# Performance work log

Measured on AMD Instinct MI355X. Metric: run time of the kernel, lower is better.

Reference implementation:

```python
import jax, jax.numpy as jnp
import numpy as np

KH, KW, PAD, G = 3, 3, 1, 4  # kernel, padding, deformable groups


def _bilinear_gather(xg, py, px):
    """xg: [B,G,C,Hin,Win]; py,px: [B,G,K,H,W] sample coords.
    Returns [B,G,C,K,H,W] with zero padding outside the image (mmcv semantics)."""
    B, Gd, C, Hin, Win = xg.shape
    y0 = jnp.floor(py)
    x0 = jnp.floor(px)
    wy1 = py - y0
    wx1 = px - x0
    wy0 = 1.0 - wy1
    wx0 = 1.0 - wx1
    xf = xg.reshape(B, Gd, C, Hin * Win)

    def gather(yi, xi):
        valid = (yi >= 0) & (yi < Hin) & (xi >= 0) & (xi < Win)
        yc = jnp.clip(yi, 0, Hin - 1).astype(jnp.int32)
        xc = jnp.clip(xi, 0, Win - 1).astype(jnp.int32)
        lin = (yc * Win + xc).reshape(B, Gd, 1, -1)  # [B,G,1,K*H*W]
        v = jnp.take_along_axis(xf, lin, axis=3).reshape(B, Gd, C, *yi.shape[2:])
        return v * valid[:, :, None].astype(xg.dtype)

    return (gather(y0, x0) * (wy0 * wx0)[:, :, None]
            + gather(y0, x0 + 1) * (wy0 * wx1)[:, :, None]
            + gather(y0 + 1, x0) * (wy1 * wx0)[:, :, None]
            + gather(y0 + 1, x0 + 1) * (wy1 * wx1)[:, :, None])


def setup_inputs() -> dict:
    key = jax.random.key(0)
    k1, k2, k3, k4 = jax.random.split(key, 4)
    B, Cin, Cout, H, W = 8, 256, 256, 64, 64
    x = jax.random.normal(k1, (B, Cin, H, W), dtype=jnp.float32)
    shape = jax.random.normal(k2, (B, 4, H, W), dtype=jnp.float32)
    # conv_offset: 1x1 conv, 4 -> G*2*KH*KW = 72 channels, no bias
    w_offset = jax.random.normal(k3, (G * 2 * KH * KW, 4), dtype=jnp.float32) * 0.1
    # conv_adaption: deform conv weight, no bias
    w_deform = jax.random.normal(k4, (Cout, Cin, KH, KW), dtype=jnp.float32) * 0.01
    return {"x": x, "shape": shape, "w_offset": w_offset, "w_deform": w_deform}


def reference(x, shape, w_offset, w_deform):
    B, Cin, H, W = x.shape
    Cout = w_deform.shape[0]
    K = KH * KW
    # 1x1 offset-predicting conv on detached shape
    shape = jax.lax.stop_gradient(shape)
    offset = jnp.einsum('oc,bchw->bohw', w_offset, shape)  # [B, G*2*K, H, W]
    off = offset.reshape(B, G, K, 2, H, W)  # mmcv layout: (dy, dx) per tap
    dy, dx = off[:, :, :, 0], off[:, :, :, 1]  # [B,G,K,H,W]
    # base sampling grid for each kernel tap
    ky, kx = jnp.meshgrid(jnp.arange(KH), jnp.arange(KW), indexing='ij')
    ky = ky.reshape(-1)
    kx = kx.reshape(-1)
    base_y = (ky - PAD)[:, None, None] + jnp.arange(H)[None, :, None]  # [K,H,1]
    base_x = (kx - PAD)[:, None, None] + jnp.arange(W)[None, None, :]  # [K,1,W]
    py = base_y[None, None].astype(x.dtype) + dy  # [B,G,K,H,W]
    px = base_x[None, None].astype(x.dtype) + dx
    xg = x.reshape(B, G, Cin // G, H, W)
    sampled = _bilinear_gather(xg, py, px)  # [B,G,Cpg,K,H,W]
    wr = w_deform.reshape(Cout, G, Cin // G, K)
    out = jnp.einsum('ogck,bgckhw->bohw', wr, sampled)
    return jax.nn.relu(out)
```

## Files before the change

### kernel.cpp

```cpp
#include <hip/hip_runtime.h>
#include <hip/hip_bf16.h>


#define Bn   8
#define CIN  256
#define COUT 256
#define Hn   64
#define Wn   64
#define Gn   4
#define Kn   9
#define CPG  64
#define GK   36

typedef __bf16 bf16x8 __attribute__((ext_vector_type(8)));
typedef float  f32x4  __attribute__((ext_vector_type(4)));
typedef _Float16 f16x2 __attribute__((ext_vector_type(2)));

#define SWPAD 1156
__global__ void fa_prep(const float* __restrict__ x, const float* __restrict__ w,
                        __bf16* __restrict__ xt, __bf16* __restrict__ wfrag) {
    const int bid = blockIdx.x, t = threadIdx.x;
    __shared__ __bf16 sw[16 * SWPAD];
    if (bid < 4096) {
        const int c8q = bid & 7, hwt = (bid >> 3) & 63, b = bid >> 9;
        const int hw = hwt * 64 + (t & 63);
        const int c8 = c8q * 4 + (t >> 6);
        const float* xp = x + ((size_t)(b * CIN + c8 * 8) << 12) + hw;
        bf16x8 v;
#pragma unroll
        for (int j = 0; j < 8; j++) v[j] = (__bf16)xp[(size_t)j << 12];
        *(bf16x8*)&xt[(((size_t)b << 12) + hw) * 256 + c8 * 8] = v;
    } else {
        const int mt = (bid - 4096) >> 1, gh = (bid - 4096) & 1;
        const int o0 = mt * 16, g0 = gh * 2;
        const int r = t >> 4, tr = t & 15;
        const float* wp = w + (size_t)(o0 + r) * (CIN * Kn) + g0 * (CPG * Kn);
#pragma unroll
        for (int it = 0; it < 18; it++) {
            int off = it * 64 + tr * 4;
            float4 v = *(const float4*)(wp + off);
            __bf16* d = &sw[r * SWPAD + off];
            d[0] = (__bf16)v.x; d[1] = (__bf16)v.y;
            d[2] = (__bf16)v.z; d[3] = (__bf16)v.w;
        }
        __syncthreads();
#pragma unroll
        for (int it = 0; it < 9; it++) {
            int chunk = it * 256 + t;
            int lane = chunk & 63, ks = (chunk >> 6) & 1, gkl = chunk >> 7;
            int gl = gkl / Kn, k = gkl - gl * Kn;
            int gk = g0 * Kn + gkl;
            int ol = lane & 15;
            int cbase = ks * 32 + (lane >> 4) * 8;
            bf16x8 v;
#pragma unroll
            for (int j = 0; j < 8; j++)
                v[j] = sw[ol * SWPAD + (gl * CPG + cbase + j) * Kn + k];
            *(bf16x8*)&wfrag[(((size_t)gk * 16 + mt) * 2 + ks) * 512 + lane * 8] = v;
        }
    }
}

__global__ __launch_bounds__(512, 4)
void fa_main(const __bf16* __restrict__ xt, const float* __restrict__ shp,
             const float* __restrict__ w_off, const __bf16* __restrict__ wfrag,
             float* __restrict__ out) {
    const int blk = blockIdx.x;
    const int bp = blk >> 7, h = (blk >> 1) & 63, wh = blk & 1;
    const int w0 = wh * 32;
    const int t = threadIdx.x;
    const int wid = t >> 6, lane = t & 63;
    const int col = lane & 15, quad = lane >> 4;
    const int cg = t & 7, nl = (t >> 3) & 63;

    __shared__ __align__(16) int4 s_meta[GK * 64];
    __shared__ __align__(16) __bf16 sB[2][64 * 64];
    __shared__ float s_shp[2 * 4 * 32];
    __shared__ float s_woff[GK * 8];

    if (t < 256) {
        int bb = t >> 7, c = (t >> 5) & 3, wl = t & 31;
        s_shp[t] = shp[(((bp * 2 + bb) * 4 + c) << 12) + h * Wn + w0 + wl];
    }
    for (int u = t; u < GK * 8; u += 512) s_woff[u] = w_off[u];
    __syncthreads();

    for (int i = t; i < GK * 64; i += 512) {
        int gk = i >> 6, n = i & 63;
        int bb = n >> 5, wl = n & 31;
        int g = gk / Kn, k = gk - g * Kn;
        int ky = k / 3, kx = k - ky * 3;
        float dy = 0.f, dx = 0.f;
#pragma unroll
        for (int c = 0; c < 4; c++) {
            float sv = s_shp[(bb * 4 + c) * 32 + wl];
            dy = fmaf(s_woff[gk * 8 + c],     sv, dy);
            dx = fmaf(s_woff[gk * 8 + 4 + c], sv, dx);
        }
        float py = (float)(h + ky - 1) + dy;
        float px = (float)(w0 + wl + kx - 1) + dx;
        float y0 = floorf(py), x0 = floorf(px);
        float fy = py - y0, fx = px - x0;
        int iy = (int)y0, ix = (int)x0;
        bool y0v = (unsigned)iy       < (unsigned)Hn;
        bool y1v = (unsigned)(iy + 1) < (unsigned)Hn;
        bool x0v = (unsigned)ix       < (unsigned)Wn;
        bool x1v = (unsigned)(ix + 1) < (unsigned)Wn;
        int yc0 = min(max(iy, 0), Hn - 1), yc1 = min(max(iy + 1, 0), Hn - 1);
        int xc0 = min(max(ix, 0), Wn - 1), xc1 = min(max(ix + 1, 0), Wn - 1);
        int l00 = yc0 * Wn + xc0, l01 = yc0 * Wn + xc1;
        int l10 = yc1 * Wn + xc0, l11 = yc1 * Wn + xc1;
        float wy1 = fy, wy0 = 1.f - fy, wx1 = fx, wx0 = 1.f - fx;
        float w00 = (y0v && x0v) ? wy0 * wx0 : 0.f;
        float w01 = (y0v && x1v) ? wy0 * wx1 : 0.f;
        float w10 = (y1v && x0v) ? wy1 * wx0 : 0.f;
        float w11 = (y1v && x1v) ? wy1 * wx1 : 0.f;
        f16x2 p0, p1;
        p0.x = (_Float16)w00; p0.y = (_Float16)w01;
        p1.x = (_Float16)w10; p1.y = (_Float16)w11;
        s_meta[i] = make_int4(l00 | (l01 << 16), l10 | (l11 << 16),
                              __builtin_bit_cast(int, p0),
                              __builtin_bit_cast(int, p1));
    }

    bf16x8 c4[4];
    int2   amv;

    auto issue = [&](int gk) {
        int4 mv = s_meta[gk * 64 + nl];
        amv.x = mv.z; amv.y = mv.w;
        int b = bp * 2 + (nl >> 5);
        int g = gk / Kn;
        const __bf16* base = xt + (((size_t)b << 12)) * 256 + g * CPG + cg * 8;
        c4[0] = *(const bf16x8*)(base + (size_t)(mv.x & 0xffff) * 256);
        c4[1] = *(const bf16x8*)(base + (size_t)((unsigned)mv.x >> 16) * 256);
        c4[2] = *(const bf16x8*)(base + (size_t)(mv.y & 0xffff) * 256);
        c4[3] = *(const bf16x8*)(base + (size_t)((unsigned)mv.y >> 16) * 256);
    };
    auto commit = [&](int buf) {
        f16x2 h0 = __builtin_bit_cast(f16x2, amv.x);
        f16x2 h1 = __builtin_bit_cast(f16x2, amv.y);
        float w00 = (float)h0.x, w01 = (float)h0.y;
        float w10 = (float)h1.x, w11 = (float)h1.y;
        bf16x8 r;
#pragma unroll
        for (int j = 0; j < 8; j++) {
            float v = w00 * (float)c4[0][j] + w01 * (float)c4[1][j]
                    + w10 * (float)c4[2][j] + w11 * (float)c4[3][j];
            r[j] = (__bf16)v;
        }
        *(bf16x8*)&sB[buf][(nl * 8 + (cg ^ (nl & 7))) * 8] = r;
    };

    f32x4 acc[2][4];
#pragma unroll
    for (int mt = 0; mt < 2; mt++)
#pragma unroll
        for (int nt = 0; nt < 4; nt++) acc[mt][nt] = (f32x4){0.f, 0.f, 0.f, 0.f};

    __syncthreads();

    issue(0);
    commit(0);
    issue(1);
    __syncthreads();

    for (int gk = 0; gk < GK; gk++) {
        const int buf = gk & 1;
        const __bf16* wbase = wfrag + (((size_t)gk * 16 + wid * 2) * 2) * 512;
        bf16x8 af[2][2];
#pragma unroll
        for (int ks = 0; ks < 2; ks++)
#pragma unroll
            for (int mt = 0; mt < 2; mt++)
                af[ks][mt] = *(const bf16x8*)(wbase + ((size_t)(mt * 2 + ks) * 64 + lane) * 8);
        if (gk + 1 < GK) commit(buf ^ 1);
        if (gk + 2 < GK) issue(gk + 2);
#pragma unroll
        for (int ks = 0; ks < 2; ks++) {
            bf16x8 bfv[4];
#pragma unroll
            for (int nt = 0; nt < 4; nt++) {
                int n = nt * 16 + col;
                int cq8 = ks * 4 + quad;
                bfv[nt] = *(const bf16x8*)&sB[buf][(n * 8 + (cq8 ^ (n & 7))) * 8];
            }
#pragma unroll
            for (int mt = 0; mt < 2; mt++)
#pragma unroll
                for (int nt = 0; nt < 4; nt++)
                    acc[mt][nt] = __builtin_amdgcn_mfma_f32_16x16x32_bf16(
                        af[ks][mt], bfv[nt], acc[mt][nt], 0, 0, 0);
        }
        __syncthreads();
    }

#pragma unroll
    for (int mt = 0; mt < 2; mt++)
#pragma unroll
        for (int r = 0; r < 4; r++) {
            int o = wid * 32 + mt * 16 + quad * 4 + r;
#pragma unroll
            for (int nt = 0; nt < 4; nt++) {
                int n = nt * 16 + col;
                int b = bp * 2 + (n >> 5);
                int w = w0 + (n & 31);
                out[(((size_t)(b * COUT + o)) << 12) + h * Wn + w] =
                    fmaxf(acc[mt][nt][r], 0.f);
            }
        }
}

extern "C" void kernel_launch(void* const* d_in, const int* in_sizes, int n_in,
                              void* d_out, int out_size, void* d_ws, size_t ws_size,
                              hipStream_t stream) {
    const float* x     = (const float*)d_in[0];
    const float* shp   = (const float*)d_in[1];
    const float* w_off = (const float*)d_in[2];
    const float* w_def = (const float*)d_in[3];
    float* out = (float*)d_out;
    __bf16* wfrag = (__bf16*)d_ws;
    __bf16* xt    = (__bf16*)((char*)d_ws + (2u << 20));

    fa_prep<<<4096 + 32, 256, 0, stream>>>(x, w_def, xt, wfrag);
    fa_main<<<512, 512, 0, stream>>>(xt, shp, w_off, wfrag, out);
}
```

Baseline: 146.4 us.

## Switch to fp16 with packed bilinear math, LDS-transposed prep, and reordered LDS reads

Changes the transposed input and weight fragments from bf16 to fp16. The bilinear blend now runs in packed half-precision multiply-adds instead of per-element float converts, and the MFMA becomes the f16 variant. The prep kernel's x transpose now goes through a swizzled shared-memory tile with coalesced float4 reads and 16-byte writes. The main loop hoists all B-fragment LDS reads ahead of the commit/issue step and uses 32-bit index arithmetic for gathers. Accumulating the blend in fp16 and the narrower fp16 exponent range could cost accuracy.

```diff
diff --git a/kernel.cpp b/kernel.cpp
--- a/kernel.cpp
+++ b/kernel.cpp
@@ -12,26 +12,44 @@
 #define CPG  64
 #define GK   36
 
-typedef __bf16 bf16x8 __attribute__((ext_vector_type(8)));
-typedef float  f32x4  __attribute__((ext_vector_type(4)));
+typedef float    f32x4 __attribute__((ext_vector_type(4)));
 typedef _Float16 f16x2 __attribute__((ext_vector_type(2)));
+typedef _Float16 f16x8 __attribute__((ext_vector_type(8)));
 
 #define SWPAD 1156
+#define HWT   32
 __global__ void fa_prep(const float* __restrict__ x, const float* __restrict__ w,
-                        __bf16* __restrict__ xt, __bf16* __restrict__ wfrag) {
+                        _Float16* __restrict__ xt, _Float16* __restrict__ wfrag) {
     const int bid = blockIdx.x, t = threadIdx.x;
-    __shared__ __bf16 sw[16 * SWPAD];
-    if (bid < 4096) {
-        const int c8q = bid & 7, hwt = (bid >> 3) & 63, b = bid >> 9;
-        const int hw = hwt * 64 + (t & 63);
-        const int c8 = c8q * 4 + (t >> 6);
-        const float* xp = x + ((size_t)(b * CIN + c8 * 8) << 12) + hw;
-        bf16x8 v;
-#pragma unroll
-        for (int j = 0; j < 8; j++) v[j] = (__bf16)xp[(size_t)j << 12];
-        *(bf16x8*)&xt[(((size_t)b << 12) + hw) * 256 + c8 * 8] = v;
+    __shared__ __align__(16) _Float16 spool[16 * SWPAD];
+    if (bid < 1024) {
+        _Float16* sT = spool;
+        const int b = bid >> 7, tile = bid & 127;
+        const int hw0 = tile * HWT;
+        const int s = t >> 3, hwq = t & 7;
+#pragma unroll
+        for (int it = 0; it < 8; it++) {
+            int c = it * 32 + s;
+            float4 v = *(const float4*)(x + (((size_t)(b * CIN + c)) << 12) + hw0 + hwq * 4);
+            const float* vf = (const float*)&v;
+#pragma unroll
+            for (int j = 0; j < 4; j++) {
+                int hw = hwq * 4 + j;
+                sT[hw * 256 + (c ^ (hwq << 3))] = (_Float16)vf[j];
+            }
+        }
+        __syncthreads();
+        const int cg = t & 31, hwr = t >> 5;
+#pragma unroll
+        for (int it = 0; it < 4; it++) {
+            int hw = it * 8 + hwr;
+            int q = hw >> 2;
+            f16x8 v = *(const f16x8*)&sT[hw * 256 + ((cg ^ q) << 3)];
+            *(f16x8*)&xt[(((size_t)b << 12) + hw0 + hw) * 256 + cg * 8] = v;
+        }
     } else {
-        const int mt = (bid - 4096) >> 1, gh = (bid - 4096) & 1;
+        _Float16* sw = spool;
+        const int mt = (bid - 1024) >> 1, gh = (bid - 1024) & 1;
         const int o0 = mt * 16, g0 = gh * 2;
         const int r = t >> 4, tr = t & 15;
         const float* wp = w + (size_t)(o0 + r) * (CIN * Kn) + g0 * (CPG * Kn);
@@ -39,9 +57,9 @@
         for (int it = 0; it < 18; it++) {
             int off = it * 64 + tr * 4;
             float4 v = *(const float4*)(wp + off);
-            __bf16* d = &sw[r * SWPAD + off];
-            d[0] = (__bf16)v.x; d[1] = (__bf16)v.y;
-            d[2] = (__bf16)v.z; d[3] = (__bf16)v.w;
+            _Float16* d = &sw[r * SWPAD + off];
+            d[0] = (_Float16)v.x; d[1] = (_Float16)v.y;
+            d[2] = (_Float16)v.z; d[3] = (_Float16)v.w;
         }
         __syncthreads();
 #pragma unroll
@@ -52,18 +70,18 @@
             int gk = g0 * Kn + gkl;
             int ol = lane & 15;
             int cbase = ks * 32 + (lane >> 4) * 8;
-            bf16x8 v;
+            f16x8 v;
 #pragma unroll
             for (int j = 0; j < 8; j++)
                 v[j] = sw[ol * SWPAD + (gl * CPG + cbase + j) * Kn + k];
-            *(bf16x8*)&wfrag[(((size_t)gk * 16 + mt) * 2 + ks) * 512 + lane * 8] = v;
+            *(f16x8*)&wfrag[(((size_t)gk * 16 + mt) * 2 + ks) * 512 + lane * 8] = v;
         }
     }
 }
 
 __global__ __launch_bounds__(512, 4)
-void fa_main(const __bf16* __restrict__ xt, const float* __restrict__ shp,
-             const float* __restrict__ w_off, const __bf16* __restrict__ wfrag,
+void fa_main(const _Float16* __restrict__ xt, const float* __restrict__ shp,
+             const float* __restrict__ w_off, const _Float16* __restrict__ wfrag,
              float* __restrict__ out) {
     const int blk = blockIdx.x;
     const int bp = blk >> 7, h = (blk >> 1) & 63, wh = blk & 1;
@@ -74,7 +92,7 @@
     const int cg = t & 7, nl = (t >> 3) & 63;
 
     __shared__ __align__(16) int4 s_meta[GK * 64];
-    __shared__ __align__(16) __bf16 sB[2][64 * 64];
+    __shared__ __align__(16) _Float16 sB[2][64 * 64];
     __shared__ float s_shp[2 * 4 * 32];
     __shared__ float s_woff[GK * 8];
 
@@ -123,33 +141,40 @@
                               __builtin_bit_cast(int, p1));
     }
 
-    bf16x8 c4[4];
-    int2   amv;
+    f16x8 c4[4];
+    int2  amv;
+    const unsigned nBase = ((unsigned)(bp * 2 + (nl >> 5)) << 20) + (unsigned)cg * 8u;
 
     auto issue = [&](int gk) {
         int4 mv = s_meta[gk * 64 + nl];
         amv.x = mv.z; amv.y = mv.w;
-        int b = bp * 2 + (nl >> 5);
-        int g = gk / Kn;
-        const __bf16* base = xt + (((size_t)b << 12)) * 256 + g * CPG + cg * 8;
-        c4[0] = *(const bf16x8*)(base + (size_t)(mv.x & 0xffff) * 256);
-        c4[1] = *(const bf16x8*)(base + (size_t)((unsigned)mv.x >> 16) * 256);
-        c4[2] = *(const bf16x8*)(base + (size_t)(mv.y & 0xffff) * 256);
-        c4[3] = *(const bf16x8*)(base + (size_t)((unsigned)mv.y >> 16) * 256);
+        unsigned g = (unsigned)gk / (unsigned)Kn;
+        unsigned base = nBase + g * 64u;
+        c4[0] = *(const f16x8*)(xt + base + (((unsigned)mv.x & 0xffffu) << 8));
+        c4[1] = *(const f16x8*)(xt + base + (((unsigned)mv.x >> 16)     << 8));
+        c4[2] = *(const f16x8*)(xt + base + (((unsigned)mv.y & 0xffffu) << 8));
+        c4[3] = *(const f16x8*)(xt + base + (((unsigned)mv.y >> 16)     << 8));
     };
     auto commit = [&](int buf) {
-        f16x2 h0 = __builtin_bit_cast(f16x2, amv.x);
-        f16x2 h1 = __builtin_bit_cast(f16x2, amv.y);
-        float w00 = (float)h0.x, w01 = (float)h0.y;
-        float w10 = (float)h1.x, w11 = (float)h1.y;
-        bf16x8 r;
-#pragma unroll
-        for (int j = 0; j < 8; j++) {
-            float v = w00 * (float)c4[0][j] + w01 * (float)c4[1][j]
-                    + w10 * (float)c4[2][j] + w11 * (float)c4[3][j];
-            r[j] = (__bf16)v;
-        }
-        *(bf16x8*)&sB[buf][(nl * 8 + (cg ^ (nl & 7))) * 8] = r;
+        f16x2 wv0 = __builtin_bit_cast(f16x2, amv.x);
+        f16x2 wv1 = __builtin_bit_cast(f16x2, amv.y);
+        f16x2 w00 = __builtin_shufflevector(wv0, wv0, 0, 0);
+        f16x2 w01 = __builtin_shufflevector(wv0, wv0, 1, 1);
+        f16x2 w10 = __builtin_shufflevector(wv1, wv1, 0, 0);
+        f16x2 w11 = __builtin_shufflevector(wv1, wv1, 1, 1);
+        const f16x2* a0p = (const f16x2*)&c4[0];
+        const f16x2* a1p = (const f16x2*)&c4[1];
+        const f16x2* a2p = (const f16x2*)&c4[2];
+        const f16x2* a3p = (const f16x2*)&c4[3];
+        f16x8 r;
+        f16x2* rp = (f16x2*)&r;
+#pragma unroll
+        for (int p = 0; p < 4; p++) {
+            f16x2 rv = w00 * a0p[p] + w01 * a1p[p]
+                     + w10 * a2p[p] + w11 * a3p[p];
+            rp[p] = rv;
+        }
+        *(f16x8*)&sB[buf][(nl * 8 + (cg ^ (nl & 7))) * 8] = r;
     };
 
     f32x4 acc[2][4];
@@ -167,31 +192,32 @@
 
     for (int gk = 0; gk < GK; gk++) {
         const int buf = gk & 1;
-        const __bf16* wbase = wfrag + (((size_t)gk * 16 + wid * 2) * 2) * 512;
-        bf16x8 af[2][2];
+        const _Float16* wbase = wfrag + (((size_t)gk * 16 + wid * 2) * 2) * 512;
+        f16x8 af[2][2];
 #pragma unroll
         for (int ks = 0; ks < 2; ks++)
 #pragma unroll
             for (int mt = 0; mt < 2; mt++)
-                af[ks][mt] = *(const bf16x8*)(wbase + ((size_t)(mt * 2 + ks) * 64 + lane) * 8);
-        if (gk + 1 < GK) commit(buf ^ 1);
-        if (gk + 2 < GK) issue(gk + 2);
-#pragma unroll
-        for (int ks = 0; ks < 2; ks++) {
-            bf16x8 bfv[4];
+                af[ks][mt] = *(const f16x8*)(wbase + ((size_t)(mt * 2 + ks) * 64 + lane) * 8);
+        f16x8 bfv[2][4];
+#pragma unroll
+        for (int ks = 0; ks < 2; ks++)
 #pragma unroll
             for (int nt = 0; nt < 4; nt++) {
                 int n = nt * 16 + col;
                 int cq8 = ks * 4 + quad;
-                bfv[nt] = *(const bf16x8*)&sB[buf][(n * 8 + (cq8 ^ (n & 7))) * 8];
+                bfv[ks][nt] = *(const f16x8*)&sB[buf][(n * 8 + (cq8 ^ (n & 7))) * 8];
             }
+        if (gk + 1 < GK) commit(buf ^ 1);
+        if (gk + 2 < GK) issue(gk + 2);
+#pragma unroll
+        for (int ks = 0; ks < 2; ks++)
 #pragma unroll
             for (int mt = 0; mt < 2; mt++)
 #pragma unroll
                 for (int nt = 0; nt < 4; nt++)
-                    acc[mt][nt] = __builtin_amdgcn_mfma_f32_16x16x32_bf16(
-                        af[ks][mt], bfv[nt], acc[mt][nt], 0, 0, 0);
-        }
+                    acc[mt][nt] = __builtin_amdgcn_mfma_f32_16x16x32_f16(
+                        af[ks][mt], bfv[ks][nt], acc[mt][nt], 0, 0, 0);
         __syncthreads();
     }
 
@@ -219,9 +245,9 @@
     const float* w_off = (const float*)d_in[2];
     const float* w_def = (const float*)d_in[3];
     float* out = (float*)d_out;
-    __bf16* wfrag = (__bf16*)d_ws;
-    __bf16* xt    = (__bf16*)((char*)d_ws + (2u << 20));
-
-    fa_prep<<<4096 + 32, 256, 0, stream>>>(x, w_def, xt, wfrag);
+    _Float16* wfrag = (_Float16*)d_ws;
+    _Float16* xt    = (_Float16*)((char*)d_ws + (2u << 20));
+
+    fa_prep<<<1024 + 32, 256, 0, stream>>>(x, w_def, xt, wfrag);
     fa_main<<<512, 512, 0, stream>>>(xt, shp, w_off, wfrag, out);
 }
```

Measured after the change: 139.9 us. -4.5%, faster.
